# Kernel tuning notes

Measured on AMD Instinct MI355X. Metric: run time of the kernel, lower is better.

The kernel has to match this reference:

```python
import math
import jax, jax.numpy as jnp
import numpy as np

B, L, S, H, E, D = 4, 2048, 2048, 8, 64, 64

def setup_inputs() -> dict:
    key = jax.random.key(0)
    kq, kk, kv = jax.random.split(key, 3)
    return {
        "queries": jax.random.normal(kq, (B, L, H, E), dtype=jnp.float32),
        "keys": jax.random.normal(kk, (B, S, H, E), dtype=jnp.float32),
        "values": jax.random.normal(kv, (B, S, H, D), dtype=jnp.float32),
    }

def reference(queries, keys, values):
    E_ = queries.shape[-1]
    scale = 1.0 / math.sqrt(E_)
    # scores: [B, H, L, S]
    scores = jnp.einsum('blhe,bshe->bhls', queries, keys)
    A = jax.nn.softmax(scale * scores, axis=-1)
    # dropout omitted (eval mode / p=0.0)
    out = jnp.einsum('bhls,bshd->blhd', A, values)
    return out
```

## Files before the change

kernel.cpp:

```cpp
#include <hip/hip_runtime.h>
#include <hip/hip_bf16.h>


#define BNUM 4
#define LLEN 2048
#define SLEN 2048
#define HNUM 8
#define EDIM 64

typedef __attribute__((ext_vector_type(8))) short s16x8;
typedef __attribute__((ext_vector_type(8))) _Float16 hf16x8;
typedef __attribute__((ext_vector_type(2))) __fp16 fp16x2;
typedef __attribute__((ext_vector_type(4))) float f32x4;

__device__ __forceinline__ short f2h(float f) {
    union { _Float16 h; short s; } u;
    u.h = (_Float16)f;
    return u.s;
}

__device__ __forceinline__ s16x8 pk8(float4 a, float4 b) {
    union { fp16x2 h[4]; s16x8 v; } u;
    u.h[0] = __builtin_amdgcn_cvt_pkrtz(a.x, a.y);
    u.h[1] = __builtin_amdgcn_cvt_pkrtz(a.z, a.w);
    u.h[2] = __builtin_amdgcn_cvt_pkrtz(b.x, b.y);
    u.h[3] = __builtin_amdgcn_cvt_pkrtz(b.z, b.w);
    return u.v;
}

#if __has_builtin(__builtin_amdgcn_global_load_lds)
#define HAVE_GLL 1
#else
#define HAVE_GLL 0
#endif

__device__ __forceinline__ void stage16(const short* g, short* l) {
#if HAVE_GLL
    __builtin_amdgcn_global_load_lds(
        (const __attribute__((address_space(1))) void*)g,
        (__attribute__((address_space(3))) void*)l, 16, 0, 0);
#else
    *(s16x8*)l = *(const s16x8*)g;
#endif
}

__global__ __launch_bounds__(256)
void prep(const float* __restrict__ Kg, const float* __restrict__ Vg,
          short* __restrict__ Kc, short* __restrict__ Vt)
{
    __shared__ short tile[EDIM][80];
    if (blockIdx.y == 0) {
        const int t = blockIdx.x * 256 + threadIdx.x;
        const int e8 = t & 7;
        const int tmp = t >> 3;
        const int h = tmp & 7;
        const int tmp2 = tmp >> 3;
        const int s = tmp2 & (SLEN - 1);
        const int b = tmp2 >> 11;
        const float4* src = (const float4*)(Kg + (((size_t)(b * SLEN + s) * HNUM + h) * EDIM + e8 * 8));
        float4 a = src[0], bb = src[1];
        *(s16x8*)(Kc + ((size_t)((b * HNUM + h) * SLEN + s) * EDIM + e8 * 8)) = pk8(a, bb);
    } else {
        if (blockIdx.x >= 1024) return;
        const int x = blockIdx.x;
        const int s0 = (x & 31) * 64;
        const int bh = x >> 5;
        const int b = bh >> 3, h = bh & 7;
        {
            const int sr = threadIdx.x >> 2, dc = (threadIdx.x & 3) * 16;
            const float4* src = (const float4*)(Vg + (((size_t)(b * SLEN + s0 + sr) * HNUM + h) * EDIM + dc));
            #pragma unroll
            for (int j4 = 0; j4 < 4; ++j4) {
                float4 a = src[j4];
                tile[dc + j4*4 + 0][sr] = f2h(a.x);
                tile[dc + j4*4 + 1][sr] = f2h(a.y);
                tile[dc + j4*4 + 2][sr] = f2h(a.z);
                tile[dc + j4*4 + 3][sr] = f2h(a.w);
            }
        }
        __syncthreads();
        {
            const int dr = threadIdx.x >> 2, sc = (threadIdx.x & 3) * 16;
            short* dst = Vt + ((size_t)((b * HNUM + h) * EDIM + dr) * SLEN + s0 + sc);
            *(s16x8*)dst       = *(const s16x8*)&tile[dr][sc];
            *(s16x8*)(dst + 8) = *(const s16x8*)&tile[dr][sc + 8];
        }
    }
}

__global__ __launch_bounds__(128, 2)
void fa_fwd(const float* __restrict__ Qg, const short* __restrict__ Kc,
            const short* __restrict__ Vt, float* __restrict__ Og)
{
    __shared__ short sKV[8704];
    __shared__ float sL[2][64];

    const int tid  = threadIdx.x;
    const int wave = tid >> 6;
    const int lane = tid & 63;
    const int m    = lane & 15;
    const int quad = lane >> 4;

    const int lin  = (int)blockIdx.x;
    const int logi = ((lin & 7) << 7) + (lin >> 3);
    const int qx = logi & 31;
    const int h  = (logi >> 5) & 7;
    const int b  = logi >> 8;
    const int qbase = qx * 64;
    const int bh = b * HNUM + h;

    const short* Kbh = Kc + (size_t)bh * SLEN * EDIM;
    const short* Vbh = Vt + (size_t)bh * EDIM * SLEN;

    const int l3 = lane >> 3;
    const int ksrcE = (wave * 32 + l3) * EDIM + ((lane & 7) ^ (l3 & 3)) * 8;
    const int ksrcO = (wave * 32 + l3) * EDIM + ((lane & 7) ^ (4 + (l3 & 3))) * 8;
    const int vsrcB = (lane >> 2) * SLEN + wave * 32 + ((lane & 3) ^ ((lane >> 2) & 3)) * 8;
    short* kdstB = sKV + (wave * 256 + lane) * 8;
    short* vdstB = sKV + 4096 + (wave * 256 + lane) * 8;

#define STAGE_TILE(s0)                                                        \
    do {                                                                      \
        _Pragma("unroll")                                                     \
        for (int p = 0; p < 4; ++p) {                                         \
            const int ks = ((p & 1) ? ksrcO : ksrcE) + (p >> 1) * 1024 + (p & 1) * 512; \
            stage16(Kbh + (size_t)(s0) * EDIM + ks, kdstB + p * 512);         \
            stage16(Vbh + (s0) + vsrcB + p * 16 * SLEN, vdstB + p * 512);     \
        }                                                                     \
    } while (0)

    const float csc = 0.18033688011112042f;
    hf16x8 qfrag[4][2];
    #pragma unroll
    for (int qt = 0; qt < 4; ++qt)
        #pragma unroll
        for (int kb = 0; kb < 2; ++kb) {
            const float* qp = Qg + ((size_t)(b * LLEN + qbase + qt * 16 + m) * HNUM + h) * EDIM
                              + kb * 32 + quad * 8;
            float4 x0 = *(const float4*)qp;
            float4 x1 = *(const float4*)(qp + 4);
            float4 y0 = {x0.x*csc, x0.y*csc, x0.z*csc, x0.w*csc};
            float4 y1 = {x1.x*csc, x1.y*csc, x1.z*csc, x1.w*csc};
            union { s16x8 s; hf16x8 h; } u;
            u.s = pk8(y0, y1);
            qfrag[qt][kb] = u.h;
        }

    const int gk  = ((m >> 2) & 1) * 4 + (m & 3);
    const int pi0 = 8 * (m >> 2) + (m & 3);
    const int kOff00 = (wave * 32 + pi0)     * 64 + ((quad)     ^ gk) * 8;
    const int kOff01 = (wave * 32 + pi0)     * 64 + ((4 + quad) ^ gk) * 8;
    const int kOff10 = (wave * 32 + pi0 + 4) * 64 + ((quad)     ^ gk) * 8;
    const int kOff11 = (wave * 32 + pi0 + 4) * 64 + ((4 + quad) ^ gk) * 8;
    const int vOffB  = 4096 + wave * 2048 + m * 32 + ((quad ^ (m & 3)) * 8);

    hf16x8 vones;
    #pragma unroll
    for (int j = 0; j < 8; ++j) vones[j] = (_Float16)1.0f;

    f32x4 oacc[4][4];
    f32x4 lacc[4];
    #pragma unroll
    for (int i = 0; i < 4; ++i) {
        #pragma unroll
        for (int j = 0; j < 4; ++j) oacc[i][j] = (f32x4){0.f, 0.f, 0.f, 0.f};
        lacc[i] = (f32x4){0.f, 0.f, 0.f, 0.f};
    }

    STAGE_TILE(0);
    __syncthreads();

    for (int s0 = 0; s0 < SLEN; s0 += 64) {
        hf16x8 kf00 = *(const hf16x8*)(sKV + kOff00);
        hf16x8 kf01 = *(const hf16x8*)(sKV + kOff01);
        hf16x8 kf10 = *(const hf16x8*)(sKV + kOff10);
        hf16x8 kf11 = *(const hf16x8*)(sKV + kOff11);
        hf16x8 vf0 = *(const hf16x8*)(sKV + vOffB);
        hf16x8 vf1 = *(const hf16x8*)(sKV + vOffB + 512);
        hf16x8 vf2 = *(const hf16x8*)(sKV + vOffB + 1024);
        hf16x8 vf3 = *(const hf16x8*)(sKV + vOffB + 1536);

        __syncthreads();

        if (s0 + 64 < SLEN) STAGE_TILE(s0 + 64);

        #pragma unroll
        for (int qt = 0; qt < 4; ++qt) {
            f32x4 a0 = {0.f, 0.f, 0.f, 0.f};
            f32x4 a1 = {0.f, 0.f, 0.f, 0.f};
            a0 = __builtin_amdgcn_mfma_f32_16x16x32_f16(kf00, qfrag[qt][0], a0, 0, 0, 0);
            a0 = __builtin_amdgcn_mfma_f32_16x16x32_f16(kf01, qfrag[qt][1], a0, 0, 0, 0);
            a1 = __builtin_amdgcn_mfma_f32_16x16x32_f16(kf10, qfrag[qt][0], a1, 0, 0, 0);
            a1 = __builtin_amdgcn_mfma_f32_16x16x32_f16(kf11, qfrag[qt][1], a1, 0, 0, 0);
            float p0 = __builtin_amdgcn_exp2f(a0[0]);
            float p1 = __builtin_amdgcn_exp2f(a0[1]);
            float p2 = __builtin_amdgcn_exp2f(a0[2]);
            float p3 = __builtin_amdgcn_exp2f(a0[3]);
            float p4 = __builtin_amdgcn_exp2f(a1[0]);
            float p5 = __builtin_amdgcn_exp2f(a1[1]);
            float p6 = __builtin_amdgcn_exp2f(a1[2]);
            float p7 = __builtin_amdgcn_exp2f(a1[3]);
            union { fp16x2 h2[4]; hf16x8 v; } pu;
            pu.h2[0] = __builtin_amdgcn_cvt_pkrtz(p0, p1);
            pu.h2[1] = __builtin_amdgcn_cvt_pkrtz(p2, p3);
            pu.h2[2] = __builtin_amdgcn_cvt_pkrtz(p4, p5);
            pu.h2[3] = __builtin_amdgcn_cvt_pkrtz(p6, p7);
            hf16x8 pf = pu.v;
            lacc[qt] = __builtin_amdgcn_mfma_f32_16x16x32_f16(pf, vones, lacc[qt], 0, 0, 0);
            oacc[qt][0] = __builtin_amdgcn_mfma_f32_16x16x32_f16(pf, vf0, oacc[qt][0], 0, 0, 0);
            oacc[qt][1] = __builtin_amdgcn_mfma_f32_16x16x32_f16(pf, vf1, oacc[qt][1], 0, 0, 0);
            oacc[qt][2] = __builtin_amdgcn_mfma_f32_16x16x32_f16(pf, vf2, oacc[qt][2], 0, 0, 0);
            oacc[qt][3] = __builtin_amdgcn_mfma_f32_16x16x32_f16(pf, vf3, oacc[qt][3], 0, 0, 0);
        }

        __syncthreads();
    }

    if (m == 0) {
        #pragma unroll
        for (int qt = 0; qt < 4; ++qt)
            #pragma unroll
            for (int r = 0; r < 4; ++r)
                sL[wave][qt * 16 + quad * 4 + r] = lacc[qt][r];
    }
    __syncthreads();

    float* sO = (float*)sKV;
    if (wave == 0) {
        #pragma unroll
        for (int qt = 0; qt < 4; ++qt)
            #pragma unroll
            for (int dt = 0; dt < 4; ++dt)
                #pragma unroll
                for (int r = 0; r < 4; ++r)
                    sO[(qt * 16 + quad * 4 + r) * 68 + dt * 16 + m] = oacc[qt][dt][r];
    }
    __syncthreads();
    if (wave == 1) {
        #pragma unroll
        for (int qt = 0; qt < 4; ++qt)
            #pragma unroll
            for (int dt = 0; dt < 4; ++dt)
                #pragma unroll
                for (int r = 0; r < 4; ++r)
                    sO[(qt * 16 + quad * 4 + r) * 68 + dt * 16 + m] += oacc[qt][dt][r];
    }
    __syncthreads();

    {
        const int q = tid >> 1;
        const int dcol = (tid & 1) * 32;
        const float l = sL[0][q] + sL[1][q];
        const float inv = 1.0f / l;
        float* orow = Og + ((size_t)(b * LLEN + qbase + q) * HNUM + h) * EDIM + dcol;
        #pragma unroll
        for (int j = 0; j < 8; ++j) {
            float4 v = *(const float4*)(sO + q * 68 + dcol + j * 4);
            v.x *= inv; v.y *= inv; v.z *= inv; v.w *= inv;
            *(float4*)(orow + j * 4) = v;
        }
    }
}

extern "C" void kernel_launch(void* const* d_in, const int* in_sizes, int n_in,
                              void* d_out, int out_size, void* d_ws, size_t ws_size,
                              hipStream_t stream) {
    const float* Q = (const float*)d_in[0];
    const float* K = (const float*)d_in[1];
    const float* V = (const float*)d_in[2];
    float* O = (float*)d_out;

    const size_t NE = (size_t)BNUM * LLEN * HNUM * EDIM;
    short* Kc = (short*)d_ws;
    short* Vt = Kc + NE;

    prep<<<dim3(2048, 2), dim3(256), 0, stream>>>(K, V, Kc, Vt);
    fa_fwd<<<dim3(1024), dim3(128), 0, stream>>>(Q, Kc, Vt, O);
}
```

Baseline: 137.2 us.

## Split query tiles across four waves per block to raise occupancy

Blocks grow from two to four waves. Each wave pair shares an S-half of the K/V tile, and each wave owns two of the four 16-row query tiles instead of all four. This halves per-wave accumulator registers and lets more waves hide latency, while staging stays on the first two waves. The cost is duplicate LDS reads of the K/V fragments by both query-half waves, and idle waves during staging.

```diff
diff --git a/kernel.cpp b/kernel.cpp
--- a/kernel.cpp
+++ b/kernel.cpp
@@ -88,7 +88,7 @@
     }
 }
 
-__global__ __launch_bounds__(128, 2)
+__global__ __launch_bounds__(256, 4)
 void fa_fwd(const float* __restrict__ Qg, const short* __restrict__ Kc,
             const short* __restrict__ Vt, float* __restrict__ Og)
 {
@@ -97,6 +97,8 @@
 
     const int tid  = threadIdx.x;
     const int wave = tid >> 6;
+    const int sw   = wave & 1;
+    const int qh   = wave >> 1;
     const int lane = tid & 63;
     const int m    = lane & 15;
     const int quad = lane >> 4;
@@ -130,44 +132,45 @@
     } while (0)
 
     const float csc = 0.18033688011112042f;
-    hf16x8 qfrag[4][2];
+    hf16x8 qfrag[2][2];
     #pragma unroll
-    for (int qt = 0; qt < 4; ++qt)
+    for (int qtl = 0; qtl < 2; ++qtl)
         #pragma unroll
         for (int kb = 0; kb < 2; ++kb) {
-            const float* qp = Qg + ((size_t)(b * LLEN + qbase + qt * 16 + m) * HNUM + h) * EDIM
+            const int qtg = qh * 2 + qtl;
+            const float* qp = Qg + ((size_t)(b * LLEN + qbase + qtg * 16 + m) * HNUM + h) * EDIM
                               + kb * 32 + quad * 8;
             float4 x0 = *(const float4*)qp;
             float4 x1 = *(const float4*)(qp + 4);
             float4 y0 = {x0.x*csc, x0.y*csc, x0.z*csc, x0.w*csc};
             float4 y1 = {x1.x*csc, x1.y*csc, x1.z*csc, x1.w*csc};
-            union { s16x8 s; hf16x8 h; } u;
+            union { s16x8 s; hf16x8 hh; } u;
             u.s = pk8(y0, y1);
-            qfrag[qt][kb] = u.h;
+            qfrag[qtl][kb] = u.hh;
         }
 
     const int gk  = ((m >> 2) & 1) * 4 + (m & 3);
     const int pi0 = 8 * (m >> 2) + (m & 3);
-    const int kOff00 = (wave * 32 + pi0)     * 64 + ((quad)     ^ gk) * 8;
-    const int kOff01 = (wave * 32 + pi0)     * 64 + ((4 + quad) ^ gk) * 8;
-    const int kOff10 = (wave * 32 + pi0 + 4) * 64 + ((quad)     ^ gk) * 8;
-    const int kOff11 = (wave * 32 + pi0 + 4) * 64 + ((4 + quad) ^ gk) * 8;
-    const int vOffB  = 4096 + wave * 2048 + m * 32 + ((quad ^ (m & 3)) * 8);
+    const int kOff00 = (sw * 32 + pi0)     * 64 + ((quad)     ^ gk) * 8;
+    const int kOff01 = (sw * 32 + pi0)     * 64 + ((4 + quad) ^ gk) * 8;
+    const int kOff10 = (sw * 32 + pi0 + 4) * 64 + ((quad)     ^ gk) * 8;
+    const int kOff11 = (sw * 32 + pi0 + 4) * 64 + ((4 + quad) ^ gk) * 8;
+    const int vOffB  = 4096 + sw * 2048 + m * 32 + ((quad ^ (m & 3)) * 8);
 
     hf16x8 vones;
     #pragma unroll
     for (int j = 0; j < 8; ++j) vones[j] = (_Float16)1.0f;
 
-    f32x4 oacc[4][4];
-    f32x4 lacc[4];
+    f32x4 oacc[2][4];
+    f32x4 lacc[2];
     #pragma unroll
-    for (int i = 0; i < 4; ++i) {
+    for (int i = 0; i < 2; ++i) {
         #pragma unroll
         for (int j = 0; j < 4; ++j) oacc[i][j] = (f32x4){0.f, 0.f, 0.f, 0.f};
         lacc[i] = (f32x4){0.f, 0.f, 0.f, 0.f};
     }
 
-    STAGE_TILE(0);
+    if (wave < 2) STAGE_TILE(0);
     __syncthreads();
 
     for (int s0 = 0; s0 < SLEN; s0 += 64) {
@@ -182,16 +185,16 @@
 
         __syncthreads();
 
-        if (s0 + 64 < SLEN) STAGE_TILE(s0 + 64);
-
-        #pragma unroll
-        for (int qt = 0; qt < 4; ++qt) {
+        if (s0 + 64 < SLEN && wave < 2) STAGE_TILE(s0 + 64);
+
+        #pragma unroll
+        for (int qtl = 0; qtl < 2; ++qtl) {
             f32x4 a0 = {0.f, 0.f, 0.f, 0.f};
             f32x4 a1 = {0.f, 0.f, 0.f, 0.f};
-            a0 = __builtin_amdgcn_mfma_f32_16x16x32_f16(kf00, qfrag[qt][0], a0, 0, 0, 0);
-            a0 = __builtin_amdgcn_mfma_f32_16x16x32_f16(kf01, qfrag[qt][1], a0, 0, 0, 0);
-            a1 = __builtin_amdgcn_mfma_f32_16x16x32_f16(kf10, qfrag[qt][0], a1, 0, 0, 0);
-            a1 = __builtin_amdgcn_mfma_f32_16x16x32_f16(kf11, qfrag[qt][1], a1, 0, 0, 0);
+            a0 = __builtin_amdgcn_mfma_f32_16x16x32_f16(kf00, qfrag[qtl][0], a0, 0, 0, 0);
+            a0 = __builtin_amdgcn_mfma_f32_16x16x32_f16(kf01, qfrag[qtl][1], a0, 0, 0, 0);
+            a1 = __builtin_amdgcn_mfma_f32_16x16x32_f16(kf10, qfrag[qtl][0], a1, 0, 0, 0);
+            a1 = __builtin_amdgcn_mfma_f32_16x16x32_f16(kf11, qfrag[qtl][1], a1, 0, 0, 0);
             float p0 = __builtin_amdgcn_exp2f(a0[0]);
             float p1 = __builtin_amdgcn_exp2f(a0[1]);
             float p2 = __builtin_amdgcn_exp2f(a0[2]);
@@ -206,11 +209,11 @@
             pu.h2[2] = __builtin_amdgcn_cvt_pkrtz(p4, p5);
             pu.h2[3] = __builtin_amdgcn_cvt_pkrtz(p6, p7);
             hf16x8 pf = pu.v;
-            lacc[qt] = __builtin_amdgcn_mfma_f32_16x16x32_f16(pf, vones, lacc[qt], 0, 0, 0);
-            oacc[qt][0] = __builtin_amdgcn_mfma_f32_16x16x32_f16(pf, vf0, oacc[qt][0], 0, 0, 0);
-            oacc[qt][1] = __builtin_amdgcn_mfma_f32_16x16x32_f16(pf, vf1, oacc[qt][1], 0, 0, 0);
-            oacc[qt][2] = __builtin_amdgcn_mfma_f32_16x16x32_f16(pf, vf2, oacc[qt][2], 0, 0, 0);
-            oacc[qt][3] = __builtin_amdgcn_mfma_f32_16x16x32_f16(pf, vf3, oacc[qt][3], 0, 0, 0);
+            lacc[qtl] = __builtin_amdgcn_mfma_f32_16x16x32_f16(pf, vones, lacc[qtl], 0, 0, 0);
+            oacc[qtl][0] = __builtin_amdgcn_mfma_f32_16x16x32_f16(pf, vf0, oacc[qtl][0], 0, 0, 0);
+            oacc[qtl][1] = __builtin_amdgcn_mfma_f32_16x16x32_f16(pf, vf1, oacc[qtl][1], 0, 0, 0);
+            oacc[qtl][2] = __builtin_amdgcn_mfma_f32_16x16x32_f16(pf, vf2, oacc[qtl][2], 0, 0, 0);
+            oacc[qtl][3] = __builtin_amdgcn_mfma_f32_16x16x32_f16(pf, vf3, oacc[qtl][3], 0, 0, 0);
         }
 
         __syncthreads();
@@ -218,43 +221,43 @@
 
     if (m == 0) {
         #pragma unroll
-        for (int qt = 0; qt < 4; ++qt)
+        for (int qtl = 0; qtl < 2; ++qtl)
             #pragma unroll
             for (int r = 0; r < 4; ++r)
-                sL[wave][qt * 16 + quad * 4 + r] = lacc[qt][r];
+                sL[sw][(qh * 2 + qtl) * 16 + quad * 4 + r] = lacc[qtl][r];
     }
     __syncthreads();
 
     float* sO = (float*)sKV;
-    if (wave == 0) {
-        #pragma unroll
-        for (int qt = 0; qt < 4; ++qt)
+    if (sw == 0) {
+        #pragma unroll
+        for (int qtl = 0; qtl < 2; ++qtl)
             #pragma unroll
             for (int dt = 0; dt < 4; ++dt)
                 #pragma unroll
                 for (int r = 0; r < 4; ++r)
-                    sO[(qt * 16 + quad * 4 + r) * 68 + dt * 16 + m] = oacc[qt][dt][r];
-    }
-    __syncthreads();
-    if (wave == 1) {
-        #pragma unroll
-        for (int qt = 0; qt < 4; ++qt)
+                    sO[((qh * 2 + qtl) * 16 + quad * 4 + r) * 68 + dt * 16 + m] = oacc[qtl][dt][r];
+    }
+    __syncthreads();
+    if (sw == 1) {
+        #pragma unroll
+        for (int qtl = 0; qtl < 2; ++qtl)
             #pragma unroll
             for (int dt = 0; dt < 4; ++dt)
                 #pragma unroll
                 for (int r = 0; r < 4; ++r)
-                    sO[(qt * 16 + quad * 4 + r) * 68 + dt * 16 + m] += oacc[qt][dt][r];
+                    sO[((qh * 2 + qtl) * 16 + quad * 4 + r) * 68 + dt * 16 + m] += oacc[qtl][dt][r];
     }
     __syncthreads();
 
     {
-        const int q = tid >> 1;
-        const int dcol = (tid & 1) * 32;
+        const int q = tid >> 2;
+        const int dcol = (tid & 3) * 16;
         const float l = sL[0][q] + sL[1][q];
         const float inv = 1.0f / l;
         float* orow = Og + ((size_t)(b * LLEN + qbase + q) * HNUM + h) * EDIM + dcol;
         #pragma unroll
-        for (int j = 0; j < 8; ++j) {
+        for (int j = 0; j < 4; ++j) {
             float4 v = *(const float4*)(sO + q * 68 + dcol + j * 4);
             v.x *= inv; v.y *= inv; v.z *= inv; v.w *= inv;
             *(float4*)(orow + j * 4) = v;
@@ -275,5 +278,5 @@
     short* Vt = Kc + NE;
 
     prep<<<dim3(2048, 2), dim3(256), 0, stream>>>(K, V, Kc, Vt);
-    fa_fwd<<<dim3(1024), dim3(128), 0, stream>>>(Q, Kc, Vt, O);
-}
+    fa_fwd<<<dim3(1024), dim3(256), 0, stream>>>(Q, Kc, Vt, O);
+}
```

After: 138.6 us. About the same (+1.0%).
